# Kernel tuning notes

Measured on AMD Instinct MI355X. Metric: run time of the kernel, lower is better.

## Reference

```python
import jax, jax.numpy as jnp
import numpy as np
from jax import lax

EPS = 1e-5
OUT_HW = 512  # origin image size for final bilinear upsample

def conv2d(x, w, pad, dil=1):
    # x: NCHW, w: OIHW
    return lax.conv_general_dilated(
        x, w, window_strides=(1, 1), padding=[(pad, pad), (pad, pad)],
        rhs_dilation=(dil, dil), dimension_numbers=('NCHW', 'OIHW', 'NCHW'))

def group_norm(x, gamma, beta, groups):
    B, C, H, W = x.shape
    xg = x.reshape(B, groups, C // groups, H, W)
    mu = jnp.mean(xg, axis=(2, 3, 4), keepdims=True)
    var = jnp.mean((xg - mu) ** 2, axis=(2, 3, 4), keepdims=True)
    xn = ((xg - mu) * lax.rsqrt(var + EPS)).reshape(B, C, H, W)
    return xn * gamma[None, :, None, None] + beta[None, :, None, None]

def mish(x):
    return x * jnp.tanh(jax.nn.softplus(x))

def setup_inputs() -> dict:
    key = jax.random.key(0)
    ks = jax.random.split(key, 8)
    s = 0.05  # keep conv outputs in a sane range
    return {
        'low_fea': jax.random.normal(ks[0], (48, 24, 128, 128), jnp.float32),
        'high_fea': jax.random.normal(ks[1], (48, 32, 128, 128), jnp.float32),
        'W_c0': jax.random.normal(ks[2], (16, 32, 1, 1), jnp.float32) * s,
        'W_c1': jax.random.normal(ks[3], (8, 8, 3, 3), jnp.float32) * s,
        'W_c2': jax.random.normal(ks[4], (8, 8, 3, 3), jnp.float32) * s,
        'g_bn': jnp.ones((16,), jnp.float32),
        'b_bn': jnp.zeros((16,), jnp.float32),
        'W_low': jax.random.normal(ks[5], (16, 24, 1, 1), jnp.float32) * s,
        'g_low': jnp.ones((16,), jnp.float32),
        'b_low': jnp.zeros((16,), jnp.float32),
        'W_ref': jax.random.normal(ks[6], (16, 16, 3, 3), jnp.float32) * s,
        'g_ref': jnp.ones((16,), jnp.float32),
        'b_ref': jnp.zeros((16,), jnp.float32),
        'W_seg': jax.random.normal(ks[7], (1, 16, 1, 1), jnp.float32) * s,
    }

def reference(low_fea, high_fea, W_c0, W_c1, W_c2, g_bn, b_bn,
              W_low, g_low, b_low, W_ref, g_ref, b_ref, W_seg):
    # DilatedParallelConvBlockD2(32, 16): 1x1 -> chunk -> (3x3 d1 | 3x3 d2) -> GN(1,16)
    in0 = conv2d(high_fea, W_c0, 0)            # [B,16,H,W]
    in1, in2 = in0[:, :8], in0[:, 8:]
    b1 = conv2d(in1, W_c1, 1, dil=1)
    b2 = conv2d(in2, W_c2, 2, dil=2)
    high = group_norm(jnp.concatenate([b1, b2], axis=1), g_bn, b_bn, groups=1)
    # up2_low 1x1 conv + GN(2,16)
    low = group_norm(conv2d(low_fea, W_low, 0), g_low, b_low, groups=2)
    # refine: Mish(high+low) -> 3x3 conv -> GN(2,16) -> Mish
    r = mish(high + low)
    r = mish(group_norm(conv2d(r, W_ref, 1), g_ref, b_ref, groups=2))
    # SegNIN 1x1 conv (dropout is identity at eval), bilinear upsample, sigmoid
    seg = conv2d(r, W_seg, 0)                  # [B,1,H,W]
    B = seg.shape[0]
    up = jax.image.resize(seg, (B, 1, OUT_HW, OUT_HW), method='bilinear')
    return jax.nn.sigmoid(up)
```

## Files before the change

kernel.cpp:

```cpp
#include <hip/hip_runtime.h>
#include <hip/hip_fp16.h>
#include <math.h>

#define BATCH 48
#define HH 128
#define WW 128
#define HW (128*128)
#define SZ (48*16*HW)
#define EPS 1e-5f

struct __align__(8)  h4 { __half2 a, b; };
struct __align__(16) h8 { __half2 a, b, c, d; };

__device__ __forceinline__ float4 h4f(h4 v) {
    float2 f0 = __half22float2(v.a), f1 = __half22float2(v.b);
    return make_float4(f0.x, f0.y, f1.x, f1.y);
}
__device__ __forceinline__ h4 f4h(float4 v) {
    h4 r; r.a = __floats2half2_rn(v.x, v.y); r.b = __floats2half2_rn(v.z, v.w); return r;
}

__device__ __forceinline__ float mishf(float v) {
    float t = __expf(fminf(v, 20.f));
    float u = t * (t + 2.f);
    return v * (u / (u + 2.f));
}

__device__ __forceinline__ void xcd_decode(int L, int bpb, int& b, int& w) {
    int xcd = L & 7;
    int j   = L >> 3;
    b = xcd + 8 * (j / bpb);
    w = j - (j / bpb) * bpb;
}

__global__ __launch_bounds__(256) void k_c0(const float* __restrict__ x,
                                            const float* __restrict__ W,
                                            const float* __restrict__ Wc1,
                                            const float* __restrict__ Wc2,
                                            const float* __restrict__ Wref,
                                            float* __restrict__ WTb,
                                            float* __restrict__ WTr,
                                            __half* __restrict__ out) {
    __shared__ float w[16*32];
    int tid = threadIdx.x;
    for (int i = tid; i < 512; i += 256) w[i] = W[i];
    if (blockIdx.x == 0) {
        for (int i = tid; i < 576; i += 256) {
            int co = i & 7; int t = i >> 3; int kyx = t % 9; int ci = t / 9;
            WTb[(ci*9 + kyx)*8 + co]       = Wc1[(co*8 + ci)*9 + kyx];
            WTb[576 + (ci*9 + kyx)*8 + co] = Wc2[(co*8 + ci)*9 + kyx];
        }
        for (int i = tid; i < 2304; i += 256) {
            int co = i & 7; int t = i >> 3; int kyx = t % 9; int cih = t / 9;
            int ci = cih & 15; int h = cih >> 4;
            WTr[((h*16 + ci)*9 + kyx)*8 + co] = Wref[((h*8 + co)*16 + ci)*9 + kyx];
        }
    }
    __syncthreads();
    int b, wblk;
    xcd_decode(blockIdx.x, 16, b, wblk);
    int off = ((wblk*256 + tid) << 2);
    const float* xb = x + (size_t)b * 32 * HW + off;
    float acc[16][4];
    #pragma unroll
    for (int c = 0; c < 16; ++c) { acc[c][0]=acc[c][1]=acc[c][2]=acc[c][3]=0.f; }
    #pragma unroll 8
    for (int ci = 0; ci < 32; ++ci) {
        float4 xv = *(const float4*)(xb + (size_t)ci * HW);
        #pragma unroll
        for (int co = 0; co < 16; ++co) {
            float wv = w[co*32 + ci];
            acc[co][0] += wv*xv.x; acc[co][1] += wv*xv.y;
            acc[co][2] += wv*xv.z; acc[co][3] += wv*xv.w;
        }
    }
    __half* ob = out + (size_t)b * 16 * HW + off;
    #pragma unroll
    for (int co = 0; co < 16; ++co)
        *(h4*)(ob + (size_t)co * HW) = f4h(make_float4(acc[co][0],acc[co][1],acc[co][2],acc[co][3]));
}

template<int D, int NCI>
__device__ __forceinline__ void dconv8(const __half* __restrict__ base,
                                       const float* __restrict__ wb,
                                       const __half* __restrict__ zh,
                                       __half* __restrict__ obase,
                                       float* __restrict__ statp,
                                       int y0, int tid) {
    int tx = tid & 15, ty = tid >> 4;
    int y  = y0 + ty;
    int xg = tx*8 - 4;
    bool mx0 = (tx > 0);
    bool mx3 = (tx < 15);
    bool my[3];
    #pragma unroll
    for (int ky = 0; ky < 3; ++ky) my[ky] = ((unsigned)(y + D*(ky-1)) < 128u);

    float acc[8][8];
    #pragma unroll
    for (int c = 0; c < 8; ++c)
        #pragma unroll
        for (int j = 0; j < 8; ++j) acc[c][j] = 0.f;

    h4 A0,A1,A2,A3, B0,B1,B2,B3, C0,C1,C2,C3;

    auto LD = [&](const __half* cb, int ky, h4& d0, h4& d1, h4& d2, h4& d3) {
        const __half* rp = cb + (y + D*(ky-1))*WW;
        bool m = my[ky];
        d0 = *(const h4*)((m && mx0) ? rp      : zh);
        d1 = *(const h4*)( m         ? rp + 4  : zh);
        d2 = *(const h4*)( m         ? rp + 8  : zh);
        d3 = *(const h4*)((m && mx3) ? rp + 12 : zh);
    };
    auto FMAG = [&](const float* wp, h4 d0, h4 d1, h4 d2, h4 d3) {
        float4 f0 = h4f(d0), f1 = h4f(d1), f2 = h4f(d2), f3 = h4f(d3);
        float u[16] = {f0.x,f0.y,f0.z,f0.w, f1.x,f1.y,f1.z,f1.w,
                       f2.x,f2.y,f2.z,f2.w, f3.x,f3.y,f3.z,f3.w};
        #pragma unroll
        for (int kx = 0; kx < 3; ++kx) {
            const float* wq = wp + kx*8;
            float w0 = wq[0], w1 = wq[1], w2 = wq[2], w3 = wq[3];
            float w4 = wq[4], w5 = wq[5], w6 = wq[6], w7 = wq[7];
            #pragma unroll
            for (int j = 0; j < 8; ++j) {
                float xv = u[4 - D + D*kx + j];
                acc[0][j] += w0*xv; acc[1][j] += w1*xv;
                acc[2][j] += w2*xv; acc[3][j] += w3*xv;
                acc[4][j] += w4*xv; acc[5][j] += w5*xv;
                acc[6][j] += w6*xv; acc[7][j] += w7*xv;
            }
        }
    };

    const __half* cb = base + xg;
    const float* wp = wb;
    LD(cb, 0, A0,A1,A2,A3);
    #pragma unroll 1
    for (int ci = 0; ci < NCI; ++ci) {
        LD(cb, 1, B0,B1,B2,B3);
        FMAG(wp,      A0,A1,A2,A3);
        LD(cb, 2, C0,C1,C2,C3);
        FMAG(wp + 24, B0,B1,B2,B3);
        if (ci + 1 < NCI) LD(cb + HW, 0, A0,A1,A2,A3);
        FMAG(wp + 48, C0,C1,C2,C3);
        cb += HW; wp += 72;
    }

    float s = 0.f, q = 0.f;
    __half* ob = obase + y*WW + tx*8;
    #pragma unroll
    for (int c = 0; c < 8; ++c) {
        h8 o;
        o.a = __floats2half2_rn(acc[c][0], acc[c][1]);
        o.b = __floats2half2_rn(acc[c][2], acc[c][3]);
        o.c = __floats2half2_rn(acc[c][4], acc[c][5]);
        o.d = __floats2half2_rn(acc[c][6], acc[c][7]);
        *(h8*)(ob + (size_t)c*HW) = o;
        #pragma unroll
        for (int j = 0; j < 8; ++j) { s += acc[c][j]; q += acc[c][j]*acc[c][j]; }
    }
    #pragma unroll
    for (int o = 32; o > 0; o >>= 1) { s += __shfl_down(s,o); q += __shfl_down(q,o); }
    if ((tid & 63) == 0) { atomicAdd(&statp[0], s); atomicAdd(&statp[1], q); }
}

__global__ __launch_bounds__(128) void k_branch5(const __half* __restrict__ in0,
                                                 const float* __restrict__ WTb,
                                                 const __half* __restrict__ zh,
                                                 __half* __restrict__ outp,
                                                 float* __restrict__ stat) {
    int b, w;
    xcd_decode(blockIdx.x, 32, b, w);
    int br = w >> 4;
    int y0 = (w & 15) << 3;
    int tid = threadIdx.x;
    if (br == 0) {
        dconv8<1,8>(in0 + (size_t)(b*16    )*HW, WTb,       zh,
                    outp + (size_t)(b*16    )*HW, stat + b*2, y0, tid);
    } else {
        dconv8<2,8>(in0 + (size_t)(b*16 + 8)*HW, WTb + 576, zh,
                    outp + (size_t)(b*16 + 8)*HW, stat + b*2, y0, tid);
    }
}

__global__ __launch_bounds__(256) void k_low(const float* __restrict__ x,
                                             const float* __restrict__ W,
                                             __half* __restrict__ outp,
                                             float* __restrict__ stat) {
    __shared__ float w[16*24];
    int tid = threadIdx.x;
    for (int i = tid; i < 384; i += 256) w[i] = W[i];
    __syncthreads();
    int b, wblk;
    xcd_decode(blockIdx.x, 16, b, wblk);
    int off = ((wblk*256 + tid) << 2);
    const float* xb = x + (size_t)b * 24 * HW + off;
    float acc[16][4];
    #pragma unroll
    for (int c = 0; c < 16; ++c) { acc[c][0]=acc[c][1]=acc[c][2]=acc[c][3]=0.f; }
    #pragma unroll 8
    for (int ci = 0; ci < 24; ++ci) {
        float4 xv = *(const float4*)(xb + (size_t)ci * HW);
        #pragma unroll
        for (int co = 0; co < 16; ++co) {
            float wv = w[co*24 + ci];
            acc[co][0] += wv*xv.x; acc[co][1] += wv*xv.y;
            acc[co][2] += wv*xv.z; acc[co][3] += wv*xv.w;
        }
    }
    __half* ob = outp + (size_t)b * 16 * HW + off;
    float s0=0.f,q0=0.f,s1=0.f,q1=0.f;
    #pragma unroll
    for (int co = 0; co < 16; ++co) {
        *(h4*)(ob + (size_t)co * HW) = f4h(make_float4(acc[co][0],acc[co][1],acc[co][2],acc[co][3]));
        #pragma unroll
        for (int j = 0; j < 4; ++j) {
            if (co < 8) { s0 += acc[co][j]; q0 += acc[co][j]*acc[co][j]; }
            else        { s1 += acc[co][j]; q1 += acc[co][j]*acc[co][j]; }
        }
    }
    #pragma unroll
    for (int o = 32; o > 0; o >>= 1) {
        s0 += __shfl_down(s0,o); q0 += __shfl_down(q0,o);
        s1 += __shfl_down(s1,o); q1 += __shfl_down(q1,o);
    }
    if ((tid & 63) == 0) {
        atomicAdd(&stat[b*4+0], s0); atomicAdd(&stat[b*4+1], q0);
        atomicAdd(&stat[b*4+2], s1); atomicAdd(&stat[b*4+3], q1);
    }
}

__global__ __launch_bounds__(256) void k_fuse(const __half* __restrict__ hp, const __half* __restrict__ lp,
                                              const float* __restrict__ gbn, const float* __restrict__ bbn,
                                              const float* __restrict__ glow, const float* __restrict__ blow,
                                              const float* __restrict__ sh, const float* __restrict__ sl,
                                              __half* __restrict__ r) {
    int b, wblk;
    xcd_decode(blockIdx.x, 128, b, wblk);
    int idx = wblk*256 + threadIdx.x;
    int p = b*262144 + (idx << 3);
    int c = idx >> 11;
    float muh = sh[b*2] * (1.f/262144.f);
    float varh = sh[b*2+1]*(1.f/262144.f) - muh*muh;
    float rsh = rsqrtf(varh + EPS);
    int gi = b*4 + (c>>3)*2;
    float mul = sl[gi] * (1.f/131072.f);
    float varl = sl[gi+1]*(1.f/131072.f) - mul*mul;
    float rsl = rsqrtf(varl + EPS);
    float ga = gbn[c]*rsh, bh = bbn[c] - muh*ga;
    float gl = glow[c]*rsl, bl = blow[c] - mul*gl;
    h8 hv = *(const h8*)(hp + (size_t)p);
    h8 lv = *(const h8*)(lp + (size_t)p);
    float2 h01 = __half22float2(hv.a), h23 = __half22float2(hv.b),
           h45 = __half22float2(hv.c), h67 = __half22float2(hv.d);
    float2 l01 = __half22float2(lv.a), l23 = __half22float2(lv.b),
           l45 = __half22float2(lv.c), l67 = __half22float2(lv.d);
    float o0 = mishf(h01.x*ga + bh + l01.x*gl + bl);
    float o1 = mishf(h01.y*ga + bh + l01.y*gl + bl);
    float o2 = mishf(h23.x*ga + bh + l23.x*gl + bl);
    float o3 = mishf(h23.y*ga + bh + l23.y*gl + bl);
    float o4 = mishf(h45.x*ga + bh + l45.x*gl + bl);
    float o5 = mishf(h45.y*ga + bh + l45.y*gl + bl);
    float o6 = mishf(h67.x*ga + bh + l67.x*gl + bl);
    float o7 = mishf(h67.y*ga + bh + l67.y*gl + bl);
    h8 ov;
    ov.a = __floats2half2_rn(o0,o1); ov.b = __floats2half2_rn(o2,o3);
    ov.c = __floats2half2_rn(o4,o5); ov.d = __floats2half2_rn(o6,o7);
    *(h8*)(r + (size_t)p) = ov;
}

__global__ __launch_bounds__(128) void k_ref5(const __half* __restrict__ rin,
                                              const float* __restrict__ WTr,
                                              const __half* __restrict__ zh,
                                              __half* __restrict__ outp,
                                              float* __restrict__ stat) {
    int b, w;
    xcd_decode(blockIdx.x, 32, b, w);
    int h  = w >> 4;
    int y0 = (w & 15) << 3;
    int tid = threadIdx.x;
    dconv8<1,16>(rin + (size_t)b*16*HW, WTr + h*1152, zh,
                 outp + (size_t)(b*16 + h*8)*HW, stat + b*4 + h*2, y0, tid);
}

__global__ __launch_bounds__(256) void k_seg(const __half* __restrict__ rp,
                                             const float* __restrict__ gref, const float* __restrict__ bref,
                                             const float* __restrict__ wseg, const float* __restrict__ sr,
                                             __half* __restrict__ seg) {
    int b, wblk;
    xcd_decode(blockIdx.x, 8, b, wblk);
    int off = ((wblk*256 + threadIdx.x) << 3);
    const __half* pb = rp + (size_t)b*16*HW + off;
    float a0=0,a1=0,a2=0,a3=0,a4=0,a5=0,a6=0,a7=0;
    #pragma unroll
    for (int c = 0; c < 16; ++c) {
        int gi = b*4 + (c>>3)*2;
        float mu = sr[gi] * (1.f/131072.f);
        float var = sr[gi+1]*(1.f/131072.f) - mu*mu;
        float rs = rsqrtf(var + EPS);
        float ga = gref[c]*rs, bb = bref[c] - mu*ga;
        float wv = wseg[c];
        h8 v = *(const h8*)(pb + (size_t)c*HW);
        float2 v01 = __half22float2(v.a), v23 = __half22float2(v.b),
               v45 = __half22float2(v.c), v67 = __half22float2(v.d);
        a0 += wv*mishf(v01.x*ga + bb); a1 += wv*mishf(v01.y*ga + bb);
        a2 += wv*mishf(v23.x*ga + bb); a3 += wv*mishf(v23.y*ga + bb);
        a4 += wv*mishf(v45.x*ga + bb); a5 += wv*mishf(v45.y*ga + bb);
        a6 += wv*mishf(v67.x*ga + bb); a7 += wv*mishf(v67.y*ga + bb);
    }
    h8 ov;
    ov.a = __floats2half2_rn(a0,a1); ov.b = __floats2half2_rn(a2,a3);
    ov.c = __floats2half2_rn(a4,a5); ov.d = __floats2half2_rn(a6,a7);
    *(h8*)(seg + (size_t)b*HW + off) = ov;
}

__global__ __launch_bounds__(256) void k_up(const __half* __restrict__ seg, float* __restrict__ out) {
    int i4 = blockIdx.x * 256 + threadIdx.x;
    int b = i4 / (512*128);
    int rem = i4 - b*(512*128);
    int y = rem >> 7; int k = rem & 127;
    const __half* sp = seg + (size_t)b * HW;
    float fy = fminf(fmaxf(0.25f*y - 0.375f, 0.f), 127.f);
    int y0 = min((int)fy, 126);
    float wy = fy - (float)y0;
    const __half* r0 = sp + y0*WW;
    const __half* r1 = r0 + WW;
    float res[4];
    #pragma unroll
    for (int j = 0; j < 4; ++j) {
        int x = k*4 + j;
        float fx = fminf(fmaxf(0.25f*x - 0.375f, 0.f), 127.f);
        int x0 = min((int)fx, 126);
        float wx = fx - (float)x0;
        float v0 = __half2float(r0[x0])*(1.f-wx) + __half2float(r0[x0+1])*wx;
        float v1 = __half2float(r1[x0])*(1.f-wx) + __half2float(r1[x0+1])*wx;
        float v = v0*(1.f-wy) + v1*wy;
        res[j] = 1.f/(1.f + __expf(-v));
    }
    *(float4*)(out + (size_t)i4*4) = make_float4(res[0],res[1],res[2],res[3]);
}

extern "C" void kernel_launch(void* const* d_in, const int* in_sizes, int n_in,
                              void* d_out, int out_size, void* d_ws, size_t ws_size,
                              hipStream_t stream) {
    const float* low  = (const float*)d_in[0];
    const float* high = (const float*)d_in[1];
    const float* Wc0  = (const float*)d_in[2];
    const float* Wc1  = (const float*)d_in[3];
    const float* Wc2  = (const float*)d_in[4];
    const float* gbn  = (const float*)d_in[5];
    const float* bbn  = (const float*)d_in[6];
    const float* Wlow = (const float*)d_in[7];
    const float* glow = (const float*)d_in[8];
    const float* blow = (const float*)d_in[9];
    const float* Wref = (const float*)d_in[10];
    const float* gref = (const float*)d_in[11];
    const float* bref = (const float*)d_in[12];
    const float* Wseg = (const float*)d_in[13];

    float* ws = (float*)d_ws;
    __half* A  = (__half*)ws;
    __half* Bb = (__half*)(ws + (size_t)SZ);
    __half* C  = (__half*)(ws + 2*(size_t)SZ);
    __half* D  = (__half*)(ws + 3*(size_t)SZ);
    float* ST = ws + 3*(size_t)SZ + (size_t)48*HW;
    float* ZB = ST + 480;
    float* WTb = ZB + 64;
    float* WTr = WTb + 1152;

    hipMemsetAsync(ST, 0, (480 + 64)*sizeof(float), stream);

    k_c0     <<<768,   256, 0, stream>>>(high, Wc0, Wc1, Wc2, Wref, WTb, WTr, A);
    k_branch5<<<1536,  128, 0, stream>>>(A, WTb, (const __half*)ZB, Bb, ST);
    k_low    <<<768,   256, 0, stream>>>(low, Wlow, C, ST + 96);
    k_fuse   <<<6144,  256, 0, stream>>>(Bb, C, gbn, bbn, glow, blow, ST, ST + 96, A);
    k_ref5   <<<1536,  128, 0, stream>>>(A, WTr, (const __half*)ZB, Bb, ST + 288);
    k_seg    <<<384,   256, 0, stream>>>(Bb, gref, bref, Wseg, ST + 288, D);
    k_up     <<<12288, 256, 0, stream>>>(D, (float*)d_out);
}
```

Measured before the change: 417.0 us.

## Halve per-thread conv tile and software-pipeline channel loads in 1x1 and 3x3 convs

The 3x3 conv helper now computes 4 output pixels per thread instead of 8, which doubles the block count for the branch and refine kernels and cuts accumulator registers. Each iteration now processes two input channels and prefetches all three rows of the next channel while the current one is being multiplied. The 1x1 conv kernels (k_c0, k_low) load four channels at a time into two double-buffered register sets. The aim is more occupancy and latency hiding for the memory-bound convs. In exchange, the narrower tiles reuse the halo less, so there are more redundant loads per output, and the extra prefetch registers add pressure.

```diff
diff --git a/kernel.cpp b/kernel.cpp
--- a/kernel.cpp
+++ b/kernel.cpp
@@ -64,16 +64,36 @@
     float acc[16][4];
     #pragma unroll
     for (int c = 0; c < 16; ++c) { acc[c][0]=acc[c][1]=acc[c][2]=acc[c][3]=0.f; }
-    #pragma unroll 8
-    for (int ci = 0; ci < 32; ++ci) {
-        float4 xv = *(const float4*)(xb + (size_t)ci * HW);
+
+    float4 A0,A1,A2,A3, B0,B1,B2,B3;
+    auto LD4 = [&](int c4, float4& d0, float4& d1, float4& d2, float4& d3) {
+        const float* p = xb + (size_t)(c4*4) * HW;
+        d0 = *(const float4*)p; d1 = *(const float4*)(p + HW);
+        d2 = *(const float4*)(p + 2*HW); d3 = *(const float4*)(p + 3*HW);
+    };
+    auto CONS = [&](int c4, float4 d0, float4 d1, float4 d2, float4 d3) {
+        float4 xv[4] = {d0, d1, d2, d3};
         #pragma unroll
-        for (int co = 0; co < 16; ++co) {
-            float wv = w[co*32 + ci];
-            acc[co][0] += wv*xv.x; acc[co][1] += wv*xv.y;
-            acc[co][2] += wv*xv.z; acc[co][3] += wv*xv.w;
-        }
-    }
+        for (int k = 0; k < 4; ++k) {
+            int ci = c4*4 + k;
+            #pragma unroll
+            for (int co = 0; co < 16; ++co) {
+                float wv = w[co*32 + ci];
+                acc[co][0] += wv*xv[k].x; acc[co][1] += wv*xv[k].y;
+                acc[co][2] += wv*xv[k].z; acc[co][3] += wv*xv[k].w;
+            }
+        }
+    };
+
+    LD4(0, A0,A1,A2,A3);
+    #pragma unroll 1
+    for (int c4 = 0; c4 < 8; c4 += 2) {
+        LD4(c4+1, B0,B1,B2,B3);
+        CONS(c4, A0,A1,A2,A3);
+        if (c4 + 2 < 8) LD4(c4+2, A0,A1,A2,A3);
+        CONS(c4+1, B0,B1,B2,B3);
+    }
+
     __half* ob = out + (size_t)b * 16 * HW + off;
     #pragma unroll
     for (int co = 0; co < 16; ++co)
@@ -81,48 +101,45 @@
 }
 
 template<int D, int NCI>
-__device__ __forceinline__ void dconv8(const __half* __restrict__ base,
+__device__ __forceinline__ void dconv4(const __half* __restrict__ base,
                                        const float* __restrict__ wb,
                                        const __half* __restrict__ zh,
                                        __half* __restrict__ obase,
                                        float* __restrict__ statp,
                                        int y0, int tid) {
-    int tx = tid & 15, ty = tid >> 4;
+    int tx = tid & 31, ty = tid >> 5;
     int y  = y0 + ty;
-    int xg = tx*8 - 4;
+    int xg = tx*4 - 4;
     bool mx0 = (tx > 0);
-    bool mx3 = (tx < 15);
+    bool mx2 = (tx < 31);
     bool my[3];
     #pragma unroll
     for (int ky = 0; ky < 3; ++ky) my[ky] = ((unsigned)(y + D*(ky-1)) < 128u);
 
-    float acc[8][8];
-    #pragma unroll
-    for (int c = 0; c < 8; ++c)
-        #pragma unroll
-        for (int j = 0; j < 8; ++j) acc[c][j] = 0.f;
-
-    h4 A0,A1,A2,A3, B0,B1,B2,B3, C0,C1,C2,C3;
-
-    auto LD = [&](const __half* cb, int ky, h4& d0, h4& d1, h4& d2, h4& d3) {
+    float acc[8][4];
+    #pragma unroll
+    for (int c = 0; c < 8; ++c) { acc[c][0]=acc[c][1]=acc[c][2]=acc[c][3]=0.f; }
+
+    h4 P0a,P0b,P0c, P1a,P1b,P1c, P2a,P2b,P2c;
+    h4 Q0a,Q0b,Q0c, Q1a,Q1b,Q1c, Q2a,Q2b,Q2c;
+
+    auto LD = [&](const __half* cb, int ky, h4& d0, h4& d1, h4& d2) {
         const __half* rp = cb + (y + D*(ky-1))*WW;
         bool m = my[ky];
-        d0 = *(const h4*)((m && mx0) ? rp      : zh);
-        d1 = *(const h4*)( m         ? rp + 4  : zh);
-        d2 = *(const h4*)( m         ? rp + 8  : zh);
-        d3 = *(const h4*)((m && mx3) ? rp + 12 : zh);
-    };
-    auto FMAG = [&](const float* wp, h4 d0, h4 d1, h4 d2, h4 d3) {
-        float4 f0 = h4f(d0), f1 = h4f(d1), f2 = h4f(d2), f3 = h4f(d3);
-        float u[16] = {f0.x,f0.y,f0.z,f0.w, f1.x,f1.y,f1.z,f1.w,
-                       f2.x,f2.y,f2.z,f2.w, f3.x,f3.y,f3.z,f3.w};
+        d0 = *(const h4*)((m && mx0) ? rp     : zh);
+        d1 = *(const h4*)( m         ? rp + 4 : zh);
+        d2 = *(const h4*)((m && mx2) ? rp + 8 : zh);
+    };
+    auto FMAG = [&](const float* wp, h4 d0, h4 d1, h4 d2) {
+        float4 f0 = h4f(d0), f1 = h4f(d1), f2 = h4f(d2);
+        float u[12] = {f0.x,f0.y,f0.z,f0.w, f1.x,f1.y,f1.z,f1.w, f2.x,f2.y,f2.z,f2.w};
         #pragma unroll
         for (int kx = 0; kx < 3; ++kx) {
             const float* wq = wp + kx*8;
             float w0 = wq[0], w1 = wq[1], w2 = wq[2], w3 = wq[3];
             float w4 = wq[4], w5 = wq[5], w6 = wq[6], w7 = wq[7];
             #pragma unroll
-            for (int j = 0; j < 8; ++j) {
+            for (int j = 0; j < 4; ++j) {
                 float xv = u[4 - D + D*kx + j];
                 acc[0][j] += w0*xv; acc[1][j] += w1*xv;
                 acc[2][j] += w2*xv; acc[3][j] += w3*xv;
@@ -134,51 +151,57 @@
 
     const __half* cb = base + xg;
     const float* wp = wb;
-    LD(cb, 0, A0,A1,A2,A3);
+    LD(cb, 0, P0a,P0b,P0c);
+    LD(cb, 1, P1a,P1b,P1c);
+    LD(cb, 2, P2a,P2b,P2c);
     #pragma unroll 1
-    for (int ci = 0; ci < NCI; ++ci) {
-        LD(cb, 1, B0,B1,B2,B3);
-        FMAG(wp,      A0,A1,A2,A3);
-        LD(cb, 2, C0,C1,C2,C3);
-        FMAG(wp + 24, B0,B1,B2,B3);
-        if (ci + 1 < NCI) LD(cb + HW, 0, A0,A1,A2,A3);
-        FMAG(wp + 48, C0,C1,C2,C3);
-        cb += HW; wp += 72;
+    for (int ci = 0; ci < NCI; ci += 2) {
+        const __half* cb1 = cb + HW;
+        const __half* cb2 = cb + 2*HW;
+        bool more = (ci + 2 < NCI);
+        LD(cb1, 0, Q0a,Q0b,Q0c);
+        FMAG(wp,       P0a,P0b,P0c);
+        LD(cb1, 1, Q1a,Q1b,Q1c);
+        FMAG(wp + 24,  P1a,P1b,P1c);
+        LD(cb1, 2, Q2a,Q2b,Q2c);
+        FMAG(wp + 48,  P2a,P2b,P2c);
+        if (more) LD(cb2, 0, P0a,P0b,P0c);
+        FMAG(wp + 72,  Q0a,Q0b,Q0c);
+        if (more) LD(cb2, 1, P1a,P1b,P1c);
+        FMAG(wp + 96,  Q1a,Q1b,Q1c);
+        if (more) LD(cb2, 2, P2a,P2b,P2c);
+        FMAG(wp + 120, Q2a,Q2b,Q2c);
+        cb += 2*HW; wp += 144;
     }
 
     float s = 0.f, q = 0.f;
-    __half* ob = obase + y*WW + tx*8;
+    __half* ob = obase + y*WW + tx*4;
     #pragma unroll
     for (int c = 0; c < 8; ++c) {
-        h8 o;
-        o.a = __floats2half2_rn(acc[c][0], acc[c][1]);
-        o.b = __floats2half2_rn(acc[c][2], acc[c][3]);
-        o.c = __floats2half2_rn(acc[c][4], acc[c][5]);
-        o.d = __floats2half2_rn(acc[c][6], acc[c][7]);
-        *(h8*)(ob + (size_t)c*HW) = o;
+        *(h4*)(ob + (size_t)c*HW) = f4h(make_float4(acc[c][0],acc[c][1],acc[c][2],acc[c][3]));
         #pragma unroll
-        for (int j = 0; j < 8; ++j) { s += acc[c][j]; q += acc[c][j]*acc[c][j]; }
+        for (int j = 0; j < 4; ++j) { s += acc[c][j]; q += acc[c][j]*acc[c][j]; }
     }
     #pragma unroll
     for (int o = 32; o > 0; o >>= 1) { s += __shfl_down(s,o); q += __shfl_down(q,o); }
     if ((tid & 63) == 0) { atomicAdd(&statp[0], s); atomicAdd(&statp[1], q); }
 }
 
-__global__ __launch_bounds__(128) void k_branch5(const __half* __restrict__ in0,
+__global__ __launch_bounds__(128) void k_branch6(const __half* __restrict__ in0,
                                                  const float* __restrict__ WTb,
                                                  const __half* __restrict__ zh,
                                                  __half* __restrict__ outp,
                                                  float* __restrict__ stat) {
     int b, w;
-    xcd_decode(blockIdx.x, 32, b, w);
-    int br = w >> 4;
-    int y0 = (w & 15) << 3;
+    xcd_decode(blockIdx.x, 64, b, w);
+    int br = w >> 5;
+    int y0 = (w & 31) << 2;
     int tid = threadIdx.x;
     if (br == 0) {
-        dconv8<1,8>(in0 + (size_t)(b*16    )*HW, WTb,       zh,
+        dconv4<1,8>(in0 + (size_t)(b*16    )*HW, WTb,       zh,
                     outp + (size_t)(b*16    )*HW, stat + b*2, y0, tid);
     } else {
-        dconv8<2,8>(in0 + (size_t)(b*16 + 8)*HW, WTb + 576, zh,
+        dconv4<2,8>(in0 + (size_t)(b*16 + 8)*HW, WTb + 576, zh,
                     outp + (size_t)(b*16 + 8)*HW, stat + b*2, y0, tid);
     }
 }
@@ -198,16 +221,36 @@
     float acc[16][4];
     #pragma unroll
     for (int c = 0; c < 16; ++c) { acc[c][0]=acc[c][1]=acc[c][2]=acc[c][3]=0.f; }
-    #pragma unroll 8
-    for (int ci = 0; ci < 24; ++ci) {
-        float4 xv = *(const float4*)(xb + (size_t)ci * HW);
+
+    float4 A0,A1,A2,A3, B0,B1,B2,B3;
+    auto LD4 = [&](int c4, float4& d0, float4& d1, float4& d2, float4& d3) {
+        const float* p = xb + (size_t)(c4*4) * HW;
+        d0 = *(const float4*)p; d1 = *(const float4*)(p + HW);
+        d2 = *(const float4*)(p + 2*HW); d3 = *(const float4*)(p + 3*HW);
+    };
+    auto CONS = [&](int c4, float4 d0, float4 d1, float4 d2, float4 d3) {
+        float4 xv[4] = {d0, d1, d2, d3};
         #pragma unroll
-        for (int co = 0; co < 16; ++co) {
-            float wv = w[co*24 + ci];
-            acc[co][0] += wv*xv.x; acc[co][1] += wv*xv.y;
-            acc[co][2] += wv*xv.z; acc[co][3] += wv*xv.w;
-        }
-    }
+        for (int k = 0; k < 4; ++k) {
+            int ci = c4*4 + k;
+            #pragma unroll
+            for (int co = 0; co < 16; ++co) {
+                float wv = w[co*24 + ci];
+                acc[co][0] += wv*xv[k].x; acc[co][1] += wv*xv[k].y;
+                acc[co][2] += wv*xv[k].z; acc[co][3] += wv*xv[k].w;
+            }
+        }
+    };
+
+    LD4(0, A0,A1,A2,A3);
+    #pragma unroll 1
+    for (int c4 = 0; c4 < 6; c4 += 2) {
+        LD4(c4+1, B0,B1,B2,B3);
+        CONS(c4, A0,A1,A2,A3);
+        if (c4 + 2 < 6) LD4(c4+2, A0,A1,A2,A3);
+        CONS(c4+1, B0,B1,B2,B3);
+    }
+
     __half* ob = outp + (size_t)b * 16 * HW + off;
     float s0=0.f,q0=0.f,s1=0.f,q1=0.f;
     #pragma unroll
@@ -269,17 +312,17 @@
     *(h8*)(r + (size_t)p) = ov;
 }
 
-__global__ __launch_bounds__(128) void k_ref5(const __half* __restrict__ rin,
+__global__ __launch_bounds__(128) void k_ref6(const __half* __restrict__ rin,
                                               const float* __restrict__ WTr,
                                               const __half* __restrict__ zh,
                                               __half* __restrict__ outp,
                                               float* __restrict__ stat) {
     int b, w;
-    xcd_decode(blockIdx.x, 32, b, w);
-    int h  = w >> 4;
-    int y0 = (w & 15) << 3;
+    xcd_decode(blockIdx.x, 64, b, w);
+    int h  = w >> 5;
+    int y0 = (w & 31) << 2;
     int tid = threadIdx.x;
-    dconv8<1,16>(rin + (size_t)b*16*HW, WTr + h*1152, zh,
+    dconv4<1,16>(rin + (size_t)b*16*HW, WTr + h*1152, zh,
                  outp + (size_t)(b*16 + h*8)*HW, stat + b*4 + h*2, y0, tid);
 }
 
@@ -371,10 +414,10 @@
     hipMemsetAsync(ST, 0, (480 + 64)*sizeof(float), stream);
 
     k_c0     <<<768,   256, 0, stream>>>(high, Wc0, Wc1, Wc2, Wref, WTb, WTr, A);
-    k_branch5<<<1536,  128, 0, stream>>>(A, WTb, (const __half*)ZB, Bb, ST);
+    k_branch6<<<3072,  128, 0, stream>>>(A, WTb, (const __half*)ZB, Bb, ST);
     k_low    <<<768,   256, 0, stream>>>(low, Wlow, C, ST + 96);
     k_fuse   <<<6144,  256, 0, stream>>>(Bb, C, gbn, bbn, glow, blow, ST, ST + 96, A);
-    k_ref5   <<<1536,  128, 0, stream>>>(A, WTr, (const __half*)ZB, Bb, ST + 288);
+    k_ref6   <<<3072,  128, 0, stream>>>(A, WTr, (const __half*)ZB, Bb, ST + 288);
     k_seg    <<<384,   256, 0, stream>>>(Bb, gref, bref, Wseg, ST + 288, D);
     k_up     <<<12288, 256, 0, stream>>>(D, (float*)d_out);
 }
```

After: 1.141 ms. +173.6%, slower.

## Pad conv input rows with zero halos and merge low-branch conv into branch kernel

Applied to the files above, without the earlier changes.

The intermediate fp16 buffers feeding the 3x3 convolutions now use a padded layout with two zero rows above and below each channel plane. The zero rows are written once by the first 1x1 conv kernel, so the dilated and refine convolutions can drop their per-row boundary masks. The separate low-feature 1x1 conv kernel is folded into the branch convolution kernel by interleaving block types. This saves one launch and lets the memory-bound low conv overlap with the compute-heavy dilated convs. The cost is a slightly larger workspace footprint and more complex indexing in the fuse kernel's output addressing.

```diff
diff --git a/kernel.cpp b/kernel.cpp
--- a/kernel.cpp
+++ b/kernel.cpp
@@ -6,6 +6,8 @@
 #define HH 128
 #define WW 128
 #define HW (128*128)
+#define PHW (132*128)
+#define PCH (16*PHW)
 #define SZ (48*16*HW)
 #define EPS 1e-5f
 
@@ -59,6 +61,18 @@
     __syncthreads();
     int b, wblk;
     xcd_decode(blockIdx.x, 16, b, wblk);
+
+    if (wblk == 0) {
+        h4 z; z.a = __floats2half2_rn(0.f, 0.f); z.b = z.a;
+        for (int i = tid; i < 2048; i += 256) {
+            int ch = i >> 7;
+            int r4 = (i >> 5) & 3;
+            int cc = (i & 31) << 2;
+            int row = (r4 < 2) ? r4 : (r4 + 128);
+            *(h4*)(out + (size_t)b*PCH + (size_t)ch*PHW + row*128 + cc) = z;
+        }
+    }
+
     int off = ((wblk*256 + tid) << 2);
     const float* xb = x + (size_t)b * 32 * HW + off;
     float acc[16][4];
@@ -74,27 +88,24 @@
             acc[co][2] += wv*xv.z; acc[co][3] += wv*xv.w;
         }
     }
-    __half* ob = out + (size_t)b * 16 * HW + off;
+    __half* ob = out + (size_t)b * PCH + 256 + off;
     #pragma unroll
     for (int co = 0; co < 16; ++co)
-        *(h4*)(ob + (size_t)co * HW) = f4h(make_float4(acc[co][0],acc[co][1],acc[co][2],acc[co][3]));
+        *(h4*)(ob + (size_t)co * PHW) = f4h(make_float4(acc[co][0],acc[co][1],acc[co][2],acc[co][3]));
 }
 
 template<int D, int NCI>
-__device__ __forceinline__ void dconv8(const __half* __restrict__ base,
-                                       const float* __restrict__ wb,
-                                       const __half* __restrict__ zh,
-                                       __half* __restrict__ obase,
-                                       float* __restrict__ statp,
-                                       int y0, int tid) {
+__device__ __forceinline__ void dconv8p(const __half* __restrict__ base,
+                                        const float* __restrict__ wb,
+                                        const __half* __restrict__ zh,
+                                        __half* __restrict__ obase,
+                                        float* __restrict__ statp,
+                                        int y0, int tid) {
     int tx = tid & 15, ty = tid >> 4;
     int y  = y0 + ty;
     int xg = tx*8 - 4;
     bool mx0 = (tx > 0);
     bool mx3 = (tx < 15);
-    bool my[3];
-    #pragma unroll
-    for (int ky = 0; ky < 3; ++ky) my[ky] = ((unsigned)(y + D*(ky-1)) < 128u);
 
     float acc[8][8];
     #pragma unroll
@@ -106,11 +117,10 @@
 
     auto LD = [&](const __half* cb, int ky, h4& d0, h4& d1, h4& d2, h4& d3) {
         const __half* rp = cb + (y + D*(ky-1))*WW;
-        bool m = my[ky];
-        d0 = *(const h4*)((m && mx0) ? rp      : zh);
-        d1 = *(const h4*)( m         ? rp + 4  : zh);
-        d2 = *(const h4*)( m         ? rp + 8  : zh);
-        d3 = *(const h4*)((m && mx3) ? rp + 12 : zh);
+        d0 = *(const h4*)(mx0 ? rp      : zh);
+        d1 = *(const h4*)(rp + 4);
+        d2 = *(const h4*)(rp + 8);
+        d3 = *(const h4*)(mx3 ? rp + 12 : zh);
     };
     auto FMAG = [&](const float* wp, h4 d0, h4 d1, h4 d2, h4 d3) {
         float4 f0 = h4f(d0), f1 = h4f(d1), f2 = h4f(d2), f3 = h4f(d3);
@@ -141,9 +151,9 @@
         FMAG(wp,      A0,A1,A2,A3);
         LD(cb, 2, C0,C1,C2,C3);
         FMAG(wp + 24, B0,B1,B2,B3);
-        if (ci + 1 < NCI) LD(cb + HW, 0, A0,A1,A2,A3);
+        if (ci + 1 < NCI) LD(cb + PHW, 0, A0,A1,A2,A3);
         FMAG(wp + 48, C0,C1,C2,C3);
-        cb += HW; wp += 72;
+        cb += PHW; wp += 72;
     }
 
     float s = 0.f, q = 0.f;
@@ -164,69 +174,70 @@
     if ((tid & 63) == 0) { atomicAdd(&statp[0], s); atomicAdd(&statp[1], q); }
 }
 
-__global__ __launch_bounds__(128) void k_branch5(const __half* __restrict__ in0,
-                                                 const float* __restrict__ WTb,
-                                                 const __half* __restrict__ zh,
-                                                 __half* __restrict__ outp,
-                                                 float* __restrict__ stat) {
+__global__ __launch_bounds__(128) void k_bl(const __half* __restrict__ in0p,
+                                            const float* __restrict__ WTb,
+                                            const __half* __restrict__ zh,
+                                            __half* __restrict__ hout,
+                                            float* __restrict__ stat_br,
+                                            const float* __restrict__ xlow,
+                                            const float* __restrict__ Wlow,
+                                            __half* __restrict__ lout,
+                                            float* __restrict__ stat_low) {
+    __shared__ float wsm[16*24];
+    int tid = threadIdx.x;
     int b, w;
-    xcd_decode(blockIdx.x, 32, b, w);
-    int br = w >> 4;
-    int y0 = (w & 15) << 3;
-    int tid = threadIdx.x;
-    if (br == 0) {
-        dconv8<1,8>(in0 + (size_t)(b*16    )*HW, WTb,       zh,
-                    outp + (size_t)(b*16    )*HW, stat + b*2, y0, tid);
+    xcd_decode(blockIdx.x, 64, b, w);
+    int type = w & 1;
+    int sub  = w >> 1;
+
+    if (type == 0) {
+        int br = sub >> 4;
+        int y0 = (sub & 15) << 3;
+        if (br == 0) {
+            dconv8p<1,8>(in0p + (size_t)b*PCH + 256,            WTb,       zh,
+                         hout + (size_t)(b*16    )*HW, stat_br + b*2, y0, tid);
+        } else {
+            dconv8p<2,8>(in0p + (size_t)b*PCH + 8*(size_t)PHW + 256, WTb + 576, zh,
+                         hout + (size_t)(b*16 + 8)*HW, stat_br + b*2, y0, tid);
+        }
     } else {
-        dconv8<2,8>(in0 + (size_t)(b*16 + 8)*HW, WTb + 576, zh,
-                    outp + (size_t)(b*16 + 8)*HW, stat + b*2, y0, tid);
-    }
-}
-
-__global__ __launch_bounds__(256) void k_low(const float* __restrict__ x,
-                                             const float* __restrict__ W,
-                                             __half* __restrict__ outp,
-                                             float* __restrict__ stat) {
-    __shared__ float w[16*24];
-    int tid = threadIdx.x;
-    for (int i = tid; i < 384; i += 256) w[i] = W[i];
-    __syncthreads();
-    int b, wblk;
-    xcd_decode(blockIdx.x, 16, b, wblk);
-    int off = ((wblk*256 + tid) << 2);
-    const float* xb = x + (size_t)b * 24 * HW + off;
-    float acc[16][4];
-    #pragma unroll
-    for (int c = 0; c < 16; ++c) { acc[c][0]=acc[c][1]=acc[c][2]=acc[c][3]=0.f; }
-    #pragma unroll 8
-    for (int ci = 0; ci < 24; ++ci) {
-        float4 xv = *(const float4*)(xb + (size_t)ci * HW);
+        for (int i = tid; i < 384; i += 128) wsm[i] = Wlow[i];
+        __syncthreads();
+        int off = ((sub*128 + tid) << 2);
+        const float* xb = xlow + (size_t)b * 24 * HW + off;
+        float acc[16][4];
+        #pragma unroll
+        for (int c = 0; c < 16; ++c) { acc[c][0]=acc[c][1]=acc[c][2]=acc[c][3]=0.f; }
+        #pragma unroll 8
+        for (int ci = 0; ci < 24; ++ci) {
+            float4 xv = *(const float4*)(xb + (size_t)ci * HW);
+            #pragma unroll
+            for (int co = 0; co < 16; ++co) {
+                float wv = wsm[co*24 + ci];
+                acc[co][0] += wv*xv.x; acc[co][1] += wv*xv.y;
+                acc[co][2] += wv*xv.z; acc[co][3] += wv*xv.w;
+            }
+        }
+        __half* ob = lout + (size_t)b * 16 * HW + off;
+        float s0=0.f,q0=0.f,s1=0.f,q1=0.f;
         #pragma unroll
         for (int co = 0; co < 16; ++co) {
-            float wv = w[co*24 + ci];
-            acc[co][0] += wv*xv.x; acc[co][1] += wv*xv.y;
-            acc[co][2] += wv*xv.z; acc[co][3] += wv*xv.w;
-        }
-    }
-    __half* ob = outp + (size_t)b * 16 * HW + off;
-    float s0=0.f,q0=0.f,s1=0.f,q1=0.f;
-    #pragma unroll
-    for (int co = 0; co < 16; ++co) {
-        *(h4*)(ob + (size_t)co * HW) = f4h(make_float4(acc[co][0],acc[co][1],acc[co][2],acc[co][3]));
-        #pragma unroll
-        for (int j = 0; j < 4; ++j) {
-            if (co < 8) { s0 += acc[co][j]; q0 += acc[co][j]*acc[co][j]; }
-            else        { s1 += acc[co][j]; q1 += acc[co][j]*acc[co][j]; }
-        }
-    }
-    #pragma unroll
-    for (int o = 32; o > 0; o >>= 1) {
-        s0 += __shfl_down(s0,o); q0 += __shfl_down(q0,o);
-        s1 += __shfl_down(s1,o); q1 += __shfl_down(q1,o);
-    }
-    if ((tid & 63) == 0) {
-        atomicAdd(&stat[b*4+0], s0); atomicAdd(&stat[b*4+1], q0);
-        atomicAdd(&stat[b*4+2], s1); atomicAdd(&stat[b*4+3], q1);
+            *(h4*)(ob + (size_t)co * HW) = f4h(make_float4(acc[co][0],acc[co][1],acc[co][2],acc[co][3]));
+            #pragma unroll
+            for (int j = 0; j < 4; ++j) {
+                if (co < 8) { s0 += acc[co][j]; q0 += acc[co][j]*acc[co][j]; }
+                else        { s1 += acc[co][j]; q1 += acc[co][j]*acc[co][j]; }
+            }
+        }
+        #pragma unroll
+        for (int o = 32; o > 0; o >>= 1) {
+            s0 += __shfl_down(s0,o); q0 += __shfl_down(q0,o);
+            s1 += __shfl_down(s1,o); q1 += __shfl_down(q1,o);
+        }
+        if ((tid & 63) == 0) {
+            atomicAdd(&stat_low[b*4+0], s0); atomicAdd(&stat_low[b*4+1], q0);
+            atomicAdd(&stat_low[b*4+2], s1); atomicAdd(&stat_low[b*4+3], q1);
+        }
     }
 }
 
@@ -240,6 +251,7 @@
     int idx = wblk*256 + threadIdx.x;
     int p = b*262144 + (idx << 3);
     int c = idx >> 11;
+    int pxin = (idx << 3) & 16383;
     float muh = sh[b*2] * (1.f/262144.f);
     float varh = sh[b*2+1]*(1.f/262144.f) - muh*muh;
     float rsh = rsqrtf(varh + EPS);
@@ -266,10 +278,10 @@
     h8 ov;
     ov.a = __floats2half2_rn(o0,o1); ov.b = __floats2half2_rn(o2,o3);
     ov.c = __floats2half2_rn(o4,o5); ov.d = __floats2half2_rn(o6,o7);
-    *(h8*)(r + (size_t)p) = ov;
-}
-
-__global__ __launch_bounds__(128) void k_ref5(const __half* __restrict__ rin,
+    *(h8*)(r + (size_t)b*PCH + (size_t)c*PHW + 256 + pxin) = ov;
+}
+
+__global__ __launch_bounds__(128) void k_refp(const __half* __restrict__ rin,
                                               const float* __restrict__ WTr,
                                               const __half* __restrict__ zh,
                                               __half* __restrict__ outp,
@@ -279,8 +291,8 @@
     int h  = w >> 4;
     int y0 = (w & 15) << 3;
     int tid = threadIdx.x;
-    dconv8<1,16>(rin + (size_t)b*16*HW, WTr + h*1152, zh,
-                 outp + (size_t)(b*16 + h*8)*HW, stat + b*4 + h*2, y0, tid);
+    dconv8p<1,16>(rin + (size_t)b*PCH + 256, WTr + h*1152, zh,
+                  outp + (size_t)(b*16 + h*8)*HW, stat + b*4 + h*2, y0, tid);
 }
 
 __global__ __launch_bounds__(256) void k_seg(const __half* __restrict__ rp,
@@ -370,11 +382,11 @@
 
     hipMemsetAsync(ST, 0, (480 + 64)*sizeof(float), stream);
 
-    k_c0     <<<768,   256, 0, stream>>>(high, Wc0, Wc1, Wc2, Wref, WTb, WTr, A);
-    k_branch5<<<1536,  128, 0, stream>>>(A, WTb, (const __half*)ZB, Bb, ST);
-    k_low    <<<768,   256, 0, stream>>>(low, Wlow, C, ST + 96);
-    k_fuse   <<<6144,  256, 0, stream>>>(Bb, C, gbn, bbn, glow, blow, ST, ST + 96, A);
-    k_ref5   <<<1536,  128, 0, stream>>>(A, WTr, (const __half*)ZB, Bb, ST + 288);
-    k_seg    <<<384,   256, 0, stream>>>(Bb, gref, bref, Wseg, ST + 288, D);
-    k_up     <<<12288, 256, 0, stream>>>(D, (float*)d_out);
-}
+    k_c0  <<<768,   256, 0, stream>>>(high, Wc0, Wc1, Wc2, Wref, WTb, WTr, A);
+    k_bl  <<<3072,  128, 0, stream>>>(A, WTb, (const __half*)ZB, Bb, ST,
+                                      low, Wlow, C, ST + 96);
+    k_fuse<<<6144,  256, 0, stream>>>(Bb, C, gbn, bbn, glow, blow, ST, ST + 96, A);
+    k_refp<<<1536,  128, 0, stream>>>(A, WTr, (const __half*)ZB, Bb, ST + 288);
+    k_seg <<<384,   256, 0, stream>>>(Bb, gref, bref, Wseg, ST + 288, D);
+    k_up  <<<12288, 256, 0, stream>>>(D, (float*)d_out);
+}
```

Result: faster. 391.3 us (-6.2%).
